# Optimization experiments

Hardware: AMD Instinct MI355X
Metric: run time of the kernel (lower is better)

Reference implementation:

```python
import jax, jax.numpy as jnp
import numpy as np

DIM = 768
HEADS = 12
HEAD_DIM = DIM // HEADS
HIDDEN = 4 * DIM
EPS = 1e-5
SCALE = HEAD_DIM ** -0.5


def _ln(x, g, b):
    mu = jnp.mean(x, axis=-1, keepdims=True)
    var = jnp.var(x, axis=-1, keepdims=True)
    return (x - mu) * jax.lax.rsqrt(var + EPS) * g + b


def setup_inputs() -> dict:
    key = jax.random.key(0)
    ks = jax.random.split(key, 10)
    s = lambda fan_in: 1.0 / np.sqrt(fan_in)
    return {
        "x": jax.random.normal(ks[0], (8, 4, 512, DIM), dtype=jnp.float32),
        "g1": jnp.ones((DIM,), jnp.float32),
        "b1": jnp.zeros((DIM,), jnp.float32),
        "Wqkv": jax.random.normal(ks[1], (DIM, 3 * DIM), jnp.float32) * s(DIM),
        "Wp": jax.random.normal(ks[2], (DIM, DIM), jnp.float32) * s(DIM),
        "bp": jnp.zeros((DIM,), jnp.float32),
        "g2": jnp.ones((DIM,), jnp.float32),
        "b2": jnp.zeros((DIM,), jnp.float32),
        "W1": jax.random.normal(ks[3], (DIM, HIDDEN), jnp.float32) * s(DIM),
        "bm1": jnp.zeros((HIDDEN,), jnp.float32),
        "W2": jax.random.normal(ks[4], (HIDDEN, DIM), jnp.float32) * s(HIDDEN),
        "bm2": jnp.zeros((DIM,), jnp.float32),
    }


def reference(x, g1, b1, Wqkv, Wp, bp, g2, b2, W1, bm1, W2, bm2):
    B, S, N, D = x.shape
    h = _ln(x, g1, b1)
    qkv = h @ Wqkv                                   # [B,S,N,3D]
    qkv = qkv.reshape(B, S, N, 3, HEADS, HEAD_DIM)
    q, k, v = (qkv[..., i, :, :] for i in range(3))  # [B,S,N,H,Dh]
    # scores over tokens N, per head
    attn = jnp.einsum("bsnhd,bsmhd->bshnm", q, k) * SCALE
    attn = jax.nn.softmax(attn, axis=-1)
    y = jnp.einsum("bshnm,bsmhd->bsnhd", attn, v).reshape(B, S, N, D)
    y = y @ Wp + bp
    x = x + y
    h2 = _ln(x, g2, b2)
    m = jax.nn.gelu(h2 @ W1 + bm1, approximate=False) @ W2 + bm2
    return x + m
```

## Files before the change

kernel.cpp:

```cpp
#include <hip/hip_runtime.h>
#include <hip/hip_bf16.h>
#include <cstdint>


typedef __bf16 bf16;
typedef bf16 bf16x8 __attribute__((ext_vector_type(8)));
typedef float f32x4 __attribute__((ext_vector_type(4)));
typedef uint32_t u32;

__device__ __forceinline__ f32x4 mfma16(bf16x8 a, bf16x8 b, f32x4 c){
  return __builtin_amdgcn_mfma_f32_16x16x32_bf16(a, b, c, 0, 0, 0);
}

__device__ __forceinline__ void gload16(const void* g, const void* l){
  __builtin_amdgcn_global_load_lds(
      (__attribute__((address_space(1))) u32*)(uintptr_t)g,
      (__attribute__((address_space(3))) u32*)(u32)(uintptr_t)l,
      16, 0, 0);
}

__global__ __launch_bounds__(256)
void transpose_cast(const float* __restrict__ W, bf16* __restrict__ Wt, int K, int N)
{
  __shared__ float t[64][65];
  int n0 = blockIdx.x * 64, k0 = blockIdx.y * 64;
  int tid = threadIdx.x;
  int c = tid & 63, r4 = tid >> 6;
#pragma unroll
  for (int i = 0; i < 16; ++i){
    int r = r4 * 16 + i;
    t[r][c] = W[(size_t)(k0 + r) * N + n0 + c];
  }
  __syncthreads();
#pragma unroll
  for (int i = 0; i < 16; ++i){
    int r = r4 * 16 + i;
    Wt[(size_t)(n0 + r) * K + k0 + c] = (bf16)t[c][r];
  }
}

__global__ __launch_bounds__(256)
void ln_kernel(const float* __restrict__ x, const float* __restrict__ g,
               const float* __restrict__ b, bf16* __restrict__ out)
{
  int row = blockIdx.x;
  int tid = threadIdx.x;
  const float* xr = x + (size_t)row * 768;
  float v0 = xr[tid], v1 = xr[tid + 256], v2 = xr[tid + 512];
  float s = v0 + v1 + v2;
  float ss = v0*v0 + v1*v1 + v2*v2;
#pragma unroll
  for (int m = 1; m < 64; m <<= 1){
    s  += __shfl_xor(s,  m, 64);
    ss += __shfl_xor(ss, m, 64);
  }
  __shared__ float red[8];
  int w = tid >> 6, l = tid & 63;
  if (l == 0){ red[w] = s; red[4 + w] = ss; }
  __syncthreads();
  s  = red[0] + red[1] + red[2] + red[3];
  ss = red[4] + red[5] + red[6] + red[7];
  float mu  = s * (1.0f / 768.0f);
  float var = ss * (1.0f / 768.0f) - mu * mu;
  float rs  = rsqrtf(var + 1e-5f);
  bf16* o = out + (size_t)row * 768;
  o[tid]       = (bf16)((v0 - mu) * rs * g[tid]       + b[tid]);
  o[tid + 256] = (bf16)((v1 - mu) * rs * g[tid + 256] + b[tid + 256]);
  o[tid + 512] = (bf16)((v2 - mu) * rs * g[tid + 512] + b[tid + 512]);
}

template<int EPI, int BMQ>
__global__ __launch_bounds__(512, 2)
void gemm256(const bf16* __restrict__ A, const bf16* __restrict__ Bt,
             const float* __restrict__ bias, const float* __restrict__ res,
             void* __restrict__ Cout, int M, int N, int K)
{
  constexpr int BM   = BMQ * 64;
  constexpr int MHN  = BMQ / 2;
  constexpr int ABUF = BM * 64;
  constexpr int BUFE = ABUF + 16384;
  extern __shared__ bf16 lds[];
  const int tid = threadIdx.x;
  const int w = tid >> 6, l = tid & 63;
  const int lr = l & 15, lg = l >> 4;
  const int wr = w >> 2, wc = w & 3;
  const int nbm = M / BM, nbn = N >> 8;
  const int nwg = nbm * nbn;
  const int cpx = nwg >> 3;
  const int bid = (int)blockIdx.x;
  const int sw  = (bid & 7) * cpx + (bid >> 3);
  const int bn = sw % nbn, bm = sw / nbn;
  const int rowA0 = bm * BM, colB0 = bn << 8;

  f32x4 acc[MHN * 4][4];
#pragma unroll
  for (int i = 0; i < MHN * 4; ++i)
#pragma unroll
    for (int j = 0; j < 4; ++j) acc[i][j] = f32x4{0.f, 0.f, 0.f, 0.f};

  const int srow = l >> 3;
  const int sg   = (l & 7) ^ srow;

  bf16* nbuf = lds;
  int   ktn  = 0;

  auto stA = [&](int q){
    bf16* dst = nbuf + q * 4096 + w * 512;
    int row = q * 64 + w * 8 + srow;
    gload16(A + (size_t)(rowA0 + row) * K + ktn + sg * 8, dst);
  };
  auto stB = [&](int nh, int j){
    int hh = j * 8 + w;
    int row0 = (hh >> 2) * 64 + nh * 32 + (hh & 3) * 8;
    bf16* dst = nbuf + ABUF + row0 * 64;
    gload16(Bt + (size_t)(colB0 + row0 + srow) * K + ktn + sg * 8, dst);
  };

  const int NT = K >> 6;

  if (BMQ == 4){
    stA(0); stA(2); stB(0,0); stB(0,1); stB(1,0); stB(1,1); stA(1); stA(3);
    asm volatile("s_waitcnt vmcnt(4)" ::: "memory");
  } else {
    stA(0); stA(1); stB(0,0); stB(0,1); stB(1,0); stB(1,1);
    asm volatile("s_waitcnt vmcnt(2)" ::: "memory");
  }
  __builtin_amdgcn_s_barrier();

  bf16x8 af[4][2];
  bf16x8 bfr[2][2][2];

#define RDA(MH)                                                               \
  _Pragma("unroll")                                                           \
  for (int fr = 0; fr < 4; ++fr)                                              \
    _Pragma("unroll")                                                         \
    for (int kk = 0; kk < 2; ++kk){                                           \
      int row = wr * (BM / 2) + (MH) * 64 + fr * 16 + lr;                     \
      af[fr][kk] = *(const bf16x8*)&Abuf[row * 64 +                           \
                     (((kk * 4 + lg) ^ (lr & 7)) << 3)];                      \
    }
#define RDB(NH)                                                               \
  _Pragma("unroll")                                                           \
  for (int fc = 0; fc < 2; ++fc)                                              \
    _Pragma("unroll")                                                         \
    for (int kk = 0; kk < 2; ++kk){                                           \
      int row = wc * 64 + (NH) * 32 + fc * 16 + lr;                           \
      bfr[NH][fc][kk] = *(const bf16x8*)&Bbuf[row * 64 +                      \
                     (((kk * 4 + lg) ^ (lr & 7)) << 3)];                      \
    }
#define MM(MH, NH)                                                            \
  __builtin_amdgcn_s_setprio(1);                                              \
  _Pragma("unroll")                                                           \
  for (int fr = 0; fr < 4; ++fr)                                              \
    _Pragma("unroll")                                                         \
    for (int fc = 0; fc < 2; ++fc)                                            \
      _Pragma("unroll")                                                       \
      for (int kk = 0; kk < 2; ++kk)                                          \
        acc[(MH) * 4 + fr][(NH) * 2 + fc] =                                   \
            mfma16(af[fr][kk], bfr[NH][fc][kk], acc[(MH) * 4 + fr][(NH) * 2 + fc]); \
  __builtin_amdgcn_s_setprio(0);

  for (int T = 0; T < NT; ++T){
    const bf16* Abuf = lds + (size_t)(T & 1) * BUFE;
    const bf16* Bbuf = Abuf + ABUF;
    nbuf = lds + (size_t)((T + 1) & 1) * BUFE;
    ktn  = (T + 1) << 6;
    const bool more = (T + 1 < NT);

    RDA(0); RDB(0);
    if (BMQ == 4){ if (more){ stA(0); stA(2); }
                   if (more) asm volatile("s_waitcnt vmcnt(4)" ::: "memory");
                   else      asm volatile("s_waitcnt vmcnt(0)" ::: "memory"); }
    else         { if (more){ stA(0); stA(1); stB(0,0); }
                   if (more) asm volatile("s_waitcnt vmcnt(3)" ::: "memory");
                   else      asm volatile("s_waitcnt vmcnt(0)" ::: "memory"); }
    MM(0, 0);
    __builtin_amdgcn_s_barrier();

    RDB(1);
    if (BMQ == 4){ if (more){ stB(0,0); stB(0,1); }
                   if (more) asm volatile("s_waitcnt vmcnt(4)" ::: "memory");
                   else      asm volatile("s_waitcnt vmcnt(0)" ::: "memory"); }
    else         { if (more){ stB(0,1); stB(1,0); stB(1,1); }
                   if (more) asm volatile("s_waitcnt vmcnt(2)" ::: "memory");
                   else      asm volatile("s_waitcnt vmcnt(0)" ::: "memory"); }
    MM(0, 1);
    __builtin_amdgcn_s_barrier();

    if (BMQ == 4){
      RDA(1);
      if (more){ stB(1,0); stB(1,1); }
      if (more) asm volatile("s_waitcnt vmcnt(4)" ::: "memory");
      else      asm volatile("s_waitcnt vmcnt(0)" ::: "memory");
      MM(1, 0);
      __builtin_amdgcn_s_barrier();

      if (more){ stA(1); stA(3); }
      if (more) asm volatile("s_waitcnt vmcnt(4)" ::: "memory");
      else      asm volatile("s_waitcnt vmcnt(0)" ::: "memory");
      MM(1, 1);
      __builtin_amdgcn_s_barrier();
    }
  }
#undef RDA
#undef RDB
#undef MM

  const size_t crow = (size_t)rowA0 + wr * (BM / 2);
  const size_t ccol = (size_t)colB0 + wc * 64;
#pragma unroll
  for (int mi = 0; mi < MHN * 4; ++mi){
#pragma unroll
    for (int ni = 0; ni < 4; ++ni){
      size_t r0 = crow + (mi >> 2) * 64 + (mi & 3) * 16 + lg * 4;
      size_t c  = ccol + (ni >> 1) * 32 + (ni & 1) * 16 + lr;
#pragma unroll
      for (int i = 0; i < 4; ++i){
        size_t r = r0 + i;
        float v = acc[mi][ni][i];
        if (EPI == 0){
          ((bf16*)Cout)[r * (size_t)N + c] = (bf16)v;
        } else if (EPI == 1){
          v += bias[c];
          v = 0.5f * v * (1.0f + erff(v * 0.70710678118654752f));
          ((bf16*)Cout)[r * (size_t)N + c] = (bf16)v;
        } else {
          v += bias[c] + res[r * (size_t)N + c];
          ((float*)Cout)[r * (size_t)N + c] = v;
        }
      }
    }
  }
}

__global__ __launch_bounds__(256)
void attn_kernel(const bf16* __restrict__ qkv, bf16* __restrict__ y)
{
  int bid = blockIdx.x;
  int qt  = bid & 7;
  int bsh = bid >> 3;
  int h = bsh % 12;
  int R = bsh / 12;
  size_t rowbase = (size_t)R * 512;
  int tid = threadIdx.x, w = tid >> 6, l = tid & 63;
  int lr = l & 15, lg = l >> 4;

  __shared__ bf16 Kl[64 * 64];
  __shared__ bf16 Vt[64 * 64];
  __shared__ bf16 Pl[4][16 * 64];

  int q0 = qt * 64 + w * 16;
  bf16x8 qf[2];
#pragma unroll
  for (int ks = 0; ks < 2; ++ks)
    qf[ks] = *(const bf16x8*)&qkv[(rowbase + q0 + lr) * 2304 + h * 64 + ks * 32 + lg * 8];

  float mi[4], li[4];
  f32x4 oa[4];
#pragma unroll
  for (int i = 0; i < 4; ++i){ mi[i] = -1e30f; li[i] = 0.f; }
#pragma unroll
  for (int dt = 0; dt < 4; ++dt) oa[dt] = f32x4{0.f, 0.f, 0.f, 0.f};

  for (int c = 0; c < 8; ++c){
    __syncthreads();
    size_t tokbase = rowbase + c * 64;
#pragma unroll
    for (int it = 0; it < 2; ++it){
      int idx = it * 256 + tid;
      int t  = idx >> 3;
      int c8 = idx & 7;
      bf16x8 kv = *(const bf16x8*)&qkv[(tokbase + t) * 2304 + 768 + h * 64 + c8 * 8];
      *(bf16x8*)&Kl[t * 64 + ((c8 ^ (t & 7)) * 8)] = kv;
      bf16x8 vv = *(const bf16x8*)&qkv[(tokbase + t) * 2304 + 1536 + h * 64 + c8 * 8];
#pragma unroll
      for (int j = 0; j < 8; ++j){
        int d = c8 * 8 + j;
        Vt[d * 64 + (((t >> 3) ^ (d & 7)) * 8) + (t & 7)] = vv[j];
      }
    }
    __syncthreads();

    f32x4 s[4];
#pragma unroll
    for (int tt = 0; tt < 4; ++tt){
      f32x4 a = f32x4{0.f, 0.f, 0.f, 0.f};
#pragma unroll
      for (int ks = 0; ks < 2; ++ks){
        int row = tt * 16 + lr;
        int c8 = ks * 4 + lg;
        bf16x8 kf = *(const bf16x8*)&Kl[row * 64 + ((c8 ^ (row & 7)) * 8)];
        a = mfma16(qf[ks], kf, a);
      }
      s[tt] = a * 0.125f;
    }

    float pr[4][4];
#pragma unroll
    for (int i = 0; i < 4; ++i){
      float rm = fmaxf(fmaxf(s[0][i], s[1][i]), fmaxf(s[2][i], s[3][i]));
#pragma unroll
      for (int mm = 1; mm < 16; mm <<= 1) rm = fmaxf(rm, __shfl_xor(rm, mm, 64));
      float mn = fmaxf(mi[i], rm);
      float corr = __expf(mi[i] - mn);
      float rs = 0.f;
#pragma unroll
      for (int tt = 0; tt < 4; ++tt){
        float p = __expf(s[tt][i] - mn);
        pr[tt][i] = p;
        rs += p;
      }
#pragma unroll
      for (int mm = 1; mm < 16; mm <<= 1) rs += __shfl_xor(rs, mm, 64);
      li[i] = li[i] * corr + rs;
#pragma unroll
      for (int dt = 0; dt < 4; ++dt) oa[dt][i] *= corr;
      mi[i] = mn;
    }

#pragma unroll
    for (int i = 0; i < 4; ++i){
      int qr = lg * 4 + i;
#pragma unroll
      for (int tt = 0; tt < 4; ++tt){
        int tok = tt * 16 + lr;
        Pl[w][qr * 64 + (((tok >> 3) ^ (qr & 7)) * 8) + (tok & 7)] = (bf16)pr[tt][i];
      }
    }
    __syncthreads();

#pragma unroll
    for (int ks = 0; ks < 2; ++ks){
      bf16x8 pf = *(const bf16x8*)&Pl[w][lr * 64 + (((ks * 4 + lg) ^ (lr & 7)) * 8)];
#pragma unroll
      for (int dt = 0; dt < 4; ++dt){
        int row = dt * 16 + lr;
        int c8 = ks * 4 + lg;
        bf16x8 vf = *(const bf16x8*)&Vt[row * 64 + ((c8 ^ (row & 7)) * 8)];
        oa[dt] = mfma16(pf, vf, oa[dt]);
      }
    }
  }

#pragma unroll
  for (int i = 0; i < 4; ++i){
    float inv = 1.0f / li[i];
    size_t r = rowbase + q0 + lg * 4 + i;
#pragma unroll
    for (int dt = 0; dt < 4; ++dt)
      y[r * 768 + h * 64 + dt * 16 + lr] = (bf16)(oa[dt][i] * inv);
  }
}

extern "C" void kernel_launch(void* const* d_in, const int* in_sizes, int n_in,
                              void* d_out, int out_size, void* d_ws, size_t ws_size,
                              hipStream_t stream)
{
  (void)in_sizes; (void)n_in; (void)out_size; (void)ws_size;
  const float* x    = (const float*)d_in[0];
  const float* g1   = (const float*)d_in[1];
  const float* b1   = (const float*)d_in[2];
  const float* Wqkv = (const float*)d_in[3];
  const float* Wp   = (const float*)d_in[4];
  const float* bp   = (const float*)d_in[5];
  const float* g2   = (const float*)d_in[6];
  const float* b2   = (const float*)d_in[7];
  const float* W1   = (const float*)d_in[8];
  const float* bm1  = (const float*)d_in[9];
  const float* W2   = (const float*)d_in[10];
  const float* bm2  = (const float*)d_in[11];
  float* out = (float*)d_out;

  hipFuncSetAttribute((const void*)gemm256<0,4>, hipFuncAttributeMaxDynamicSharedMemorySize, 131072);
  hipFuncSetAttribute((const void*)gemm256<1,4>, hipFuncAttributeMaxDynamicSharedMemorySize, 131072);
  hipFuncSetAttribute((const void*)gemm256<2,2>, hipFuncAttributeMaxDynamicSharedMemorySize, 98304);

  char* ws = (char*)d_ws;
  size_t off = 0;
  auto alloc = [&](size_t nbytes) -> void* {
    void* p = ws + off;
    off += (nbytes + 255) & ~(size_t)255;
    return p;
  };
  bf16* WqkvT = (bf16*)alloc((size_t)2304 * 768 * 2);
  bf16* WpT   = (bf16*)alloc((size_t)768 * 768 * 2);
  bf16* W1T   = (bf16*)alloc((size_t)3072 * 768 * 2);
  bf16* W2T   = (bf16*)alloc((size_t)768 * 3072 * 2);
  char* R1 = (char*)alloc((size_t)16384 * 768 * 2);
  char* R2 = (char*)alloc((size_t)16384 * 3072 * 2);
  bf16* h   = (bf16*)R1;
  bf16* yb  = (bf16*)R1;
  bf16* h2  = (bf16*)R1;
  bf16* qkv = (bf16*)R2;
  bf16* m1  = (bf16*)R2;
  float* x2 = out;

  transpose_cast<<<dim3(36, 12), dim3(256), 0, stream>>>(Wqkv, WqkvT, 768, 2304);
  transpose_cast<<<dim3(12, 12), dim3(256), 0, stream>>>(Wp,   WpT,   768, 768);
  transpose_cast<<<dim3(48, 12), dim3(256), 0, stream>>>(W1,   W1T,   768, 3072);
  transpose_cast<<<dim3(12, 48), dim3(256), 0, stream>>>(W2,   W2T,   3072, 768);

  ln_kernel<<<dim3(16384), dim3(256), 0, stream>>>(x, g1, b1, h);
  gemm256<0,4><<<dim3(576), dim3(512), 131072, stream>>>(h, WqkvT, nullptr, nullptr,
                                                         (void*)qkv, 16384, 2304, 768);
  attn_kernel<<<dim3(3072), dim3(256), 0, stream>>>(qkv, yb);
  gemm256<2,2><<<dim3(384), dim3(512), 98304, stream>>>(yb, WpT, bp, x,
                                                        (void*)x2, 16384, 768, 768);
  ln_kernel<<<dim3(16384), dim3(256), 0, stream>>>(x2, g2, b2, h2);
  gemm256<1,4><<<dim3(768), dim3(512), 131072, stream>>>(h2, W1T, bm1, nullptr,
                                                         (void*)m1, 16384, 3072, 768);
  gemm256<2,2><<<dim3(384), dim3(512), 98304, stream>>>(m1, W2T, bm2, x2,
                                                        (void*)out, 16384, 768, 3072);
}
```

Baseline: 686.3 us.

## Replace fine-grained staged prefetch with whole-tile double-buffered prefetch per K step

The GEMM main loop no longer interleaves partial A/B tile loads with sub-block MFMAs under several barriers and partial vmcnt waits. It now issues all global-to-LDS loads for the next K tile at the start of each iteration, computes the full current tile, then waits on vmcnt(0) and takes one barrier. This cuts barriers per K step from up to four to one and simplifies scheduling. In exchange the loads can no longer be waited on in pieces, and a full wait at the end of each step may expose latency if compute is short.

Result: faster. 613.9 us (-10.6%).

```diff
diff --git a/kernel.cpp b/kernel.cpp
--- a/kernel.cpp
+++ b/kernel.cpp
@@ -115,17 +115,18 @@
     bf16* dst = nbuf + ABUF + row0 * 64;
     gload16(Bt + (size_t)(colB0 + row0 + srow) * K + ktn + sg * 8, dst);
   };
+  auto stageAll = [&](){
+    if (BMQ == 4){ stA(0); stA(2); stB(0,0); stB(0,1); stB(1,0); stB(1,1); stA(1); stA(3); }
+    else         { stA(0); stA(1); stB(0,0); stB(0,1); stB(1,0); stB(1,1); }
+  };
 
   const int NT = K >> 6;
 
-  if (BMQ == 4){
-    stA(0); stA(2); stB(0,0); stB(0,1); stB(1,0); stB(1,1); stA(1); stA(3);
-    asm volatile("s_waitcnt vmcnt(4)" ::: "memory");
-  } else {
-    stA(0); stA(1); stB(0,0); stB(0,1); stB(1,0); stB(1,1);
-    asm volatile("s_waitcnt vmcnt(2)" ::: "memory");
-  }
+  stageAll();
+  asm volatile("s_waitcnt vmcnt(0)" ::: "memory");
+  __builtin_amdgcn_sched_barrier(0);
   __builtin_amdgcn_s_barrier();
+  __builtin_amdgcn_sched_barrier(0);
 
   bf16x8 af[4][2];
   bf16x8 bfr[2][2][2];
@@ -167,39 +168,23 @@
     ktn  = (T + 1) << 6;
     const bool more = (T + 1 < NT);
 
+    if (more) stageAll();
+
     RDA(0); RDB(0);
-    if (BMQ == 4){ if (more){ stA(0); stA(2); }
-                   if (more) asm volatile("s_waitcnt vmcnt(4)" ::: "memory");
-                   else      asm volatile("s_waitcnt vmcnt(0)" ::: "memory"); }
-    else         { if (more){ stA(0); stA(1); stB(0,0); }
-                   if (more) asm volatile("s_waitcnt vmcnt(3)" ::: "memory");
-                   else      asm volatile("s_waitcnt vmcnt(0)" ::: "memory"); }
     MM(0, 0);
-    __builtin_amdgcn_s_barrier();
-
     RDB(1);
-    if (BMQ == 4){ if (more){ stB(0,0); stB(0,1); }
-                   if (more) asm volatile("s_waitcnt vmcnt(4)" ::: "memory");
-                   else      asm volatile("s_waitcnt vmcnt(0)" ::: "memory"); }
-    else         { if (more){ stB(0,1); stB(1,0); stB(1,1); }
-                   if (more) asm volatile("s_waitcnt vmcnt(2)" ::: "memory");
-                   else      asm volatile("s_waitcnt vmcnt(0)" ::: "memory"); }
     MM(0, 1);
-    __builtin_amdgcn_s_barrier();
-
     if (BMQ == 4){
       RDA(1);
-      if (more){ stB(1,0); stB(1,1); }
-      if (more) asm volatile("s_waitcnt vmcnt(4)" ::: "memory");
-      else      asm volatile("s_waitcnt vmcnt(0)" ::: "memory");
       MM(1, 0);
+      MM(1, 1);
+    }
+
+    if (more){
+      asm volatile("s_waitcnt vmcnt(0)" ::: "memory");
+      __builtin_amdgcn_sched_barrier(0);
       __builtin_amdgcn_s_barrier();
-
-      if (more){ stA(1); stA(3); }
-      if (more) asm volatile("s_waitcnt vmcnt(4)" ::: "memory");
-      else      asm volatile("s_waitcnt vmcnt(0)" ::: "memory");
-      MM(1, 1);
-      __builtin_amdgcn_s_barrier();
+      __builtin_amdgcn_sched_barrier(0);
     }
   }
 #undef RDA
```
